# Optimization experiments

Hardware: AMD Instinct MI355X
Metric: run time of the kernel (lower is better)

The kernel has to match this reference:

```python
import jax, jax.numpy as jnp
import numpy as np
from jax.scipy.special import logsumexp

WORD_DIM = 512
SCRF_DIM = 256
N_TAGS = 12
ALLOWED_SPAN = 8
START_ID = 10
STOP_ID = 11
SEQ_LEN = 768
N_SPANS = 96


def _compute_scores(h, Wl, bl, Wr, br, Gl, bgl, Gr, bgr, Wt, bt, transitions):
    # h: [1, L, D] already projected by Dense
    Lc, D = h.shape[1], h.shape[2]
    scores = jnp.zeros((1, Lc, Lc, D), h.dtype)
    diag = jnp.arange(Lc)
    ht = h
    scores = scores.at[:, diag, diag].set(ht)
    for sl in range(1, min(ALLOWED_SPAN, Lc)):
        l, r = ht[:, :-1], ht[:, 1:]
        h_hat = 4.0 * jax.nn.sigmoid(l @ Wl.T + bl + r @ Wr.T + br) - 2.0
        # exp/normalize over 3 gates == softmax over gate axis
        g = (l @ Gl.T + bgl + r @ Gr.T + bgr).reshape(1, Lc - sl, 3, D)
        wgt = jax.nn.softmax(g, axis=2)
        ht = wgt[:, :, 0] * h_hat + wgt[:, :, 1] * l + wgt[:, :, 2] * r
        scores = scores.at[:, diag[:Lc - sl], diag[sl:]].set(ht)
    tagsc = scores @ Wt.T + bt  # [1, L, L, T]
    # final[b,i,j,prev,tag] = tagsc[b,i,j,tag] + transitions[prev,tag]
    return tagsc[:, :, :, None, :] + transitions[None, None, None]


def _forward_pass(s5):
    # s5: [1, L, L, T, T]; semi-Markov forward algorithm, windows of width <= ALLOWED_SPAN
    Lc, T = s5.shape[1], s5.shape[3]
    A = ALLOWED_SPAN
    i0 = jnp.arange(1, Lc + 1)
    k = jnp.arange(A)
    p = i0[:, None] - A + k[None, :]              # candidate span-start positions [L, A]
    m = p >= 0                                    # valid window mask (istarts = max(0, i-A))
    x = s5[0][jnp.clip(p, 0), (i0 - 1)[:, None]]  # [L, A, T, T] span scores ending at i-1
    buf0 = jnp.full((A, T), -10000.0, s5.dtype).at[A - 1, START_ID].set(0.0)

    def step(buf, inp):
        xi, mi = inp
        # tmp[k, prev, tag] = score + logalpha[start, prev]
        tmp = jnp.where(mi[:, None, None], xi + buf[:, :, None], -1e30)
        na = logsumexp(tmp, axis=(0, 1))  # [T]
        return jnp.concatenate([buf[1:], na[None]], axis=0), na

    _, alphas = jax.lax.scan(step, buf0, (x, m))
    return alphas[-1, :STOP_ID].sum()


def _gold_score(s5, tags):
    Lc, T = s5.shape[1], s5.shape[3]
    gf = tags[:, :, 0] * (Lc * T * T) + tags[:, :, 1] * (T * T) + tags[:, :, 2] * T + tags[:, :, 3]
    return jnp.take_along_axis(s5.reshape(1, -1), gf, axis=1).sum()


def setup_inputs() -> dict:
    key = jax.random.key(0)
    ks = jax.random.split(key, 16)
    D, W3 = SCRF_DIM, 3 * SCRF_DIM
    s = 0.05
    def w(k, shape):
        return jax.random.normal(k, shape, dtype=jnp.float32) * s
    return {
        "feats": jax.random.normal(ks[0], (1, SEQ_LEN, WORD_DIM), dtype=jnp.float32),
        "tags": jax.random.randint(ks[1], (1, N_SPANS, 4), 0, N_TAGS),
        "Wd": w(ks[2], (D, WORD_DIM)), "bd": jnp.zeros((D,), jnp.float32),
        "Wl": w(ks[3], (D, D)), "bl": jnp.zeros((D,), jnp.float32),
        "Wr": w(ks[4], (D, D)), "br": jnp.zeros((D,), jnp.float32),
        "Gl": w(ks[5], (W3, D)), "bgl": jnp.zeros((W3,), jnp.float32),
        "Gr": w(ks[6], (W3, D)), "bgr": jnp.zeros((W3,), jnp.float32),
        "Wt": w(ks[7], (N_TAGS, D)), "bt": jnp.zeros((N_TAGS,), jnp.float32),
        "transitions": w(ks[8], (N_TAGS, N_TAGS)),
    }


def reference(feats, tags, Wd, bd, Wl, bl, Wr, br, Gl, bgl, Gr, bgr, Wt, bt, transitions):
    h = feats @ Wd.T + bd  # Dense: word_dim -> scrf_dim
    s5 = _compute_scores(h, Wl, bl, Wr, br, Gl, bgl, Gr, bgr, Wt, bt, transitions)
    gold = _gold_score(s5, tags)
    logZ = _forward_pass(s5)
    return logZ - gold
```

## Files before the change

### kernel.cpp

```cpp
#include <hip/hip_runtime.h>

typedef __attribute__((ext_vector_type(8))) short short8;
typedef __attribute__((ext_vector_type(4))) float f32x4;

#define TPAD 100

__device__ __forceinline__ float bf2f(short s) {
  return __uint_as_float(((unsigned)(unsigned short)s) << 16);
}
__device__ __forceinline__ unsigned short f2bf(float f) {
  unsigned u = __float_as_uint(f);
  unsigned rounding = 0x7fffu + ((u >> 16) & 1u);
  return (unsigned short)((u + rounding) >> 16);
}

__device__ __forceinline__ void stg_f32(float* p, float v) {
  asm volatile("global_store_dword %0, %1, off sc1" :: "v"(p), "v"(v) : "memory");
}
__device__ __forceinline__ void stg_u16(unsigned short* p, unsigned short v) {
  unsigned w = v;
  asm volatile("global_store_short %0, %1, off sc1" :: "v"(p), "v"(w) : "memory");
}

#define NFLAGS 18432
__device__ __forceinline__ void flag_spin(unsigned* f, unsigned tgt) {
  unsigned n = 0;
  while (__hip_atomic_load(f, __ATOMIC_RELAXED, __HIP_MEMORY_SCOPE_AGENT) < tgt) {
    __builtin_amdgcn_s_sleep(2);
    if (++n > 2000000u) break;
  }
}
#define DRAIN() asm volatile("s_waitcnt vmcnt(0) lgkmcnt(0)" ::: "memory")

union __align__(16) SmemU {
  struct { unsigned short As[64][72]; unsigned short Ws[64][72]; float Cs[64][64]; } g;
  struct { unsigned short rows[2][8][264]; float sred[2][96]; float smu[2]; } bn;
  struct { float Bs[96 * TPAD]; float Acs[96 * TPAD]; float red[8]; } t;
  struct { float Qs[2][96 * TPAD]; float vv[4][96]; float red[8]; float redm[4]; } f;
};

__global__ void prep_kernel(const float* __restrict__ feats, const float* __restrict__ Wd,
                            const float* __restrict__ Wl, const float* __restrict__ Wr,
                            const float* __restrict__ Gl, const float* __restrict__ Gr,
                            const float* __restrict__ bl, const float* __restrict__ br,
                            const float* __restrict__ bgl, const float* __restrict__ bgr,
                            unsigned short* __restrict__ featsB, unsigned short* __restrict__ WdB,
                            unsigned short* __restrict__ WcB, float* __restrict__ bc,
                            unsigned* __restrict__ flags)
{
  int idx = blockIdx.x * 256 + threadIdx.x;
  if (idx < 393216) {
    featsB[idx] = f2bf(feats[idx]);
  } else if (idx < 524288) {
    int j = idx - 393216;
    WdB[j] = f2bf(Wd[j]);
  } else if (idx < 1048576) {
    int j = idx - 524288;
    int o = j >> 9, k = j & 511;
    float v;
    if (k < 256) v = (o < 256) ? Wl[o*256 + k] : Gl[(o-256)*256 + k];
    else { int k2 = k - 256; v = (o < 256) ? Wr[o*256 + k2] : Gr[(o-256)*256 + k2]; }
    WcB[j] = f2bf(v);
  } else if (idx < 1049600) {
    int o = idx - 1048576;
    bc[o] = (o < 256) ? bl[o] + br[o] : bgl[o-256] + bgr[o-256];
  } else {
    int j = idx - 1049600;
    if (j < NFLAGS) flags[j] = 0u;
  }
}

__device__ __forceinline__ void treelevel(SmemU& sm,
    const float* Tin, const float* Cin, float* Tout, float* Cout)
{
  const int bid = blockIdx.x;
  const int tid = threadIdx.x;
  const int wv = tid >> 6, lane = tid & 63;
  const int j = bid >> 1;
  const int cs = (bid & 1) * 48;
  const float* Ag = Tin + (size_t)(2*j) * 9216;
  const float* Bg = Tin + (size_t)(2*j + 1) * 9216;

  float4 av[9], bv[9];
  const float* ap = Ag + tid * 36;
  const float* bp = Bg + tid * 36;
  #pragma unroll
  for (int q = 0; q < 9; ++q) av[q] = *(const float4*)(ap + q*4);
  #pragma unroll
  for (int q = 0; q < 9; ++q) bv[q] = *(const float4*)(bp + q*4);
  float ma = 0.f, mb = 0.f;
  #pragma unroll
  for (int q = 0; q < 9; ++q) {
    ma = fmaxf(ma, fmaxf(fmaxf(av[q].x, av[q].y), fmaxf(av[q].z, av[q].w)));
    mb = fmaxf(mb, fmaxf(fmaxf(bv[q].x, bv[q].y), fmaxf(bv[q].z, bv[q].w)));
  }
  #pragma unroll
  for (int off = 32; off; off >>= 1) {
    ma = fmaxf(ma, __shfl_down(ma, off));
    mb = fmaxf(mb, __shfl_down(mb, off));
  }
  if (lane == 0) { sm.t.red[wv] = ma; sm.t.red[4 + wv] = mb; }
  __syncthreads();
  float fa = fmaxf(fmaxf(sm.t.red[0], sm.t.red[1]), fmaxf(sm.t.red[2], sm.t.red[3]));
  float fb = fmaxf(fmaxf(sm.t.red[4], sm.t.red[5]), fmaxf(sm.t.red[6], sm.t.red[7]));
  float ia = 1.0f / fa, ib = 1.0f / fb;

  #pragma unroll
  for (int q = 0; q < 9; ++q) {
    int e = tid*36 + q*4;
    int r = e / 96, k = e - r*96;
    float4 bb = bv[q];
    bb.x *= ib; bb.y *= ib; bb.z *= ib; bb.w *= ib;
    *(float4*)&sm.t.Bs[r*TPAD + k] = bb;
    float4 aa = av[q];
    sm.t.Acs[(k+0)*TPAD + r] = aa.x * ia;
    sm.t.Acs[(k+1)*TPAD + r] = aa.y * ia;
    sm.t.Acs[(k+2)*TPAD + r] = aa.z * ia;
    sm.t.Acs[(k+3)*TPAD + r] = aa.w * ia;
  }
  __syncthreads();

  int tr = tid >> 4, tc = tid & 15;
  int r0 = tr * 6, c0 = cs + tc * 3;
  float acc[6][3];
  #pragma unroll
  for (int i = 0; i < 6; ++i)
    #pragma unroll
    for (int m = 0; m < 3; ++m) acc[i][m] = 0.f;
  for (int k = 0; k < 96; k += 4) {
    float4 a0 = *(const float4*)&sm.t.Acs[(c0+0)*TPAD + k];
    float4 a1 = *(const float4*)&sm.t.Acs[(c0+1)*TPAD + k];
    float4 a2 = *(const float4*)&sm.t.Acs[(c0+2)*TPAD + k];
    #pragma unroll
    for (int i = 0; i < 6; ++i) {
      float4 b = *(const float4*)&sm.t.Bs[(r0+i)*TPAD + k];
      acc[i][0] += b.x*a0.x + b.y*a0.y + b.z*a0.z + b.w*a0.w;
      acc[i][1] += b.x*a1.x + b.y*a1.y + b.z*a1.z + b.w*a1.w;
      acc[i][2] += b.x*a2.x + b.y*a2.y + b.z*a2.z + b.w*a2.w;
    }
  }
  float* op = Tout + (size_t)j * 9216;
  #pragma unroll
  for (int i = 0; i < 6; ++i)
    #pragma unroll
    for (int m = 0; m < 3; ++m)
      stg_f32(&op[(size_t)(r0+i)*96 + c0 + m], acc[i][m]);
  if ((bid & 1) == 0 && tid == 0)
    stg_f32(&Cout[j], Cin[2*j] + Cin[2*j + 1] + __logf(fa) + __logf(fb));
}

__global__ __launch_bounds__(256, 2) void mega_kernel(
    const unsigned short* featsB, const unsigned short* WdB,
    const float* bd, const unsigned short* WcB, const float* bc,
    unsigned short* ht, const float* Wt, const float* bt,
    float* Bband, float* Xn, float* muv, const float* trans,
    const int* tags,
    float* T0, float* T1, float* T2, float* T3, float* T4,
    float* C0, float* C1, float* C2, float* C3, float* C4,
    float* out, unsigned* flags)
{
  __shared__ SmemU sm;
  const int bid = blockIdx.x;
  const int tid = threadIdx.x;
  const int wave = tid >> 6, lane = tid & 63;

  if (bid < 192) {
    const int p = bid % 12;
    if (bid < 48) {
      const int p0 = p * 64;
      const int n0 = (bid / 12) * 64;
      f32x4 acc[4];
      #pragma unroll
      for (int i = 0; i < 4; ++i)
        #pragma unroll
        for (int j = 0; j < 4; ++j) acc[i][j] = 0.f;
      const int lr = tid >> 3;
      const int c8 = (tid & 7) * 8;
      for (int kt = 0; kt < 8; ++kt) {
        int kb = kt * 64;
        #pragma unroll
        for (int rr = 0; rr < 64; rr += 32) {
          int row = lr + rr;
          *(short8*)(&sm.g.As[row][c8]) = *(const short8*)(featsB + (size_t)(p0 + row)*512 + kb + c8);
          *(short8*)(&sm.g.Ws[row][c8]) = *(const short8*)(WdB + (size_t)(n0 + row)*512 + kb + c8);
        }
        __syncthreads();
        int q8 = (lane >> 4) * 8;
        #pragma unroll
        for (int kk = 0; kk < 2; ++kk) {
          short8 bfr = *(const short8*)(&sm.g.Ws[wave*16 + (lane & 15)][kk*32 + q8]);
          #pragma unroll
          for (int mt = 0; mt < 4; ++mt) {
            short8 afr = *(const short8*)(&sm.g.As[mt*16 + (lane & 15)][kk*32 + q8]);
            acc[mt] = __builtin_amdgcn_mfma_f32_16x16x32_bf16(afr, bfr, acc[mt], 0, 0, 0);
          }
        }
        __syncthreads();
      }
      int o = n0 + wave*16 + (lane & 15);
      float bias = bd[o];
      #pragma unroll
      for (int mt = 0; mt < 4; ++mt)
        #pragma unroll
        for (int r = 0; r < 4; ++r) {
          int row = p0 + mt*16 + (lane >> 4)*4 + r;
          stg_u16(&ht[row*256 + o], f2bf(acc[mt][r] + bias));
        }
      DRAIN();
      __syncthreads();
      if (tid == 0) atomicAdd(&flags[(0*12 + p)*32], 1u);
    }

    for (int sl = 1; sl <= 7; ++sl) {
      unsigned tgt = (sl == 1) ? 4u : 16u;
      if (tid == 0) {
        flag_spin(&flags[((sl-1)*12 + p)*32], tgt);
        if (p < 11) flag_spin(&flags[((sl-1)*12 + p + 1)*32], tgt);
      }
      __syncthreads();
      {
        const unsigned short* htp = ht + (size_t)(sl - 1) * 196608;
        unsigned short* htn = ht + (size_t)sl * 196608;
        const int Mvalid = 768 - sl;
        const int p0 = p * 64;
        const int n0 = (bid / 12) * 16;
        f32x4 acc[4];
        #pragma unroll
        for (int i = 0; i < 4; ++i)
          #pragma unroll
          for (int j = 0; j < 4; ++j) acc[i][j] = 0.f;
        const int lr = tid >> 3;
        const int c8 = (tid & 7) * 8;
        for (int kt = 0; kt < 8; ++kt) {
          int kb = kt * 64;
          int shift = kb >> 8;
          int kcol = kb & 255;
          #pragma unroll
          for (int rr = 0; rr < 64; rr += 32) {
            int row = lr + rr;
            int grow = p0 + row + shift; if (grow > 767) grow = 767;
            *(short8*)(&sm.g.As[row][c8]) = *(const short8*)(htp + (size_t)grow*256 + kcol + c8);
            int o = (row >> 4)*256 + n0 + (row & 15);
            *(short8*)(&sm.g.Ws[row][c8]) = *(const short8*)(WcB + (size_t)o*512 + kb + c8);
          }
          __syncthreads();
          int q8 = (lane >> 4) * 8;
          #pragma unroll
          for (int kk = 0; kk < 2; ++kk) {
            short8 bfr = *(const short8*)(&sm.g.Ws[wave*16 + (lane & 15)][kk*32 + q8]);
            #pragma unroll
            for (int mt = 0; mt < 4; ++mt) {
              short8 afr = *(const short8*)(&sm.g.As[mt*16 + (lane & 15)][kk*32 + q8]);
              acc[mt] = __builtin_amdgcn_mfma_f32_16x16x32_bf16(afr, bfr, acc[mt], 0, 0, 0);
            }
          }
          __syncthreads();
        }
        #pragma unroll
        for (int mt = 0; mt < 4; ++mt)
          #pragma unroll
          for (int r = 0; r < 4; ++r)
            sm.g.Cs[mt*16 + (lane >> 4)*4 + r][wave*16 + (lane & 15)] = acc[mt][r];
        __syncthreads();

        int dl = tid & 15;
        int d = n0 + dl;
        float bz = bc[d], b0 = bc[256 + d], b1 = bc[512 + d], b2v = bc[768 + d];
        for (int pr = tid >> 4; pr < 64; pr += 16) {
          int pw = p0 + pr;
          if (pw >= Mvalid) continue;
          float z  = sm.g.Cs[pr][dl]      + bz;
          float g0 = sm.g.Cs[pr][16 + dl] + b0;
          float g1 = sm.g.Cs[pr][32 + dl] + b1;
          float g2 = sm.g.Cs[pr][48 + dl] + b2v;
          float l = bf2f((short)htp[pw*256 + d]);
          float r = bf2f((short)htp[(pw+1)*256 + d]);
          float hh = 4.f / (1.f + __expf(-z)) - 2.f;
          float mg = fmaxf(g0, fmaxf(g1, g2));
          float e0 = __expf(g0 - mg), e1 = __expf(g1 - mg), e2 = __expf(g2 - mg);
          float inv = 1.f / (e0 + e1 + e2);
          stg_u16(&htn[pw*256 + d], f2bf((e0*hh + e1*l + e2*r) * inv));
        }
      }
      DRAIN();
      __syncthreads();
      if (tid == 0) atomicAdd(&flags[(sl*12 + p)*32], 1u);
    }
  }

  for (int task = bid; task < 384; task += 256) {
    if (tid == 0) {
      int rlo = 2*task - 7; if (rlo < 0) rlo = 0;
      int tlo = rlo >> 6, thi = (2*task + 1) >> 6;
      flag_spin(&flags[(7*12 + tlo)*32], 16u);
      if (thi != tlo) flag_spin(&flags[(7*12 + thi)*32], 16u);
    }
    __syncthreads();
    const int half = tid >> 7;
    const int t2 = tid & 127;
    const int i = 2*task + 1 + half;
    for (int q = t2; q < 256; q += 128) {
      int k = q >> 5, cc = (q & 31) * 8;
      int pr = i - 8 + k;
      short8 v;
      if (pr >= 0) {
        int slx = 7 - k;
        v = *(const short8*)(ht + ((size_t)slx*768 + pr)*256 + cc);
      } else {
        #pragma unroll
        for (int j = 0; j < 8; ++j) v[j] = 0;
      }
      *(short8*)(&sm.bn.rows[half][k][cc]) = v;
    }
    __syncthreads();
    float res = -1e30f;
    if (t2 < 96) {
      int t = t2 >> 3, k = t2 & 7;
      int pr = i - 8 + k;
      if (pr >= 0) {
        float acc = 0.f;
        for (int dch = 0; dch < 256; dch += 8) {
          float4 wa = *(const float4*)(Wt + t*256 + dch);
          float4 wb = *(const float4*)(Wt + t*256 + dch + 4);
          short8 hv = *(const short8*)(&sm.bn.rows[half][k][dch]);
          acc += wa.x*bf2f(hv[0]) + wa.y*bf2f(hv[1]) + wa.z*bf2f(hv[2]) + wa.w*bf2f(hv[3])
               + wb.x*bf2f(hv[4]) + wb.y*bf2f(hv[5]) + wb.z*bf2f(hv[6]) + wb.w*bf2f(hv[7]);
        }
        res = acc + bt[t];
      }
      stg_f32(&Bband[(size_t)i*96 + t2], res);
      sm.bn.sred[half][t2] = res;
    }
    __syncthreads();
    if (t2 < 32) {
      float m = fmaxf(sm.bn.sred[half][t2],
                 fmaxf(sm.bn.sred[half][t2+32], sm.bn.sred[half][t2+64]));
      #pragma unroll
      for (int off = 16; off; off >>= 1) m = fmaxf(m, __shfl_down(m, off));
      if (t2 == 0) { stg_f32(&muv[i], m); sm.bn.smu[half] = m; }
    }
    __syncthreads();
    if (t2 < 96) stg_f32(&Xn[(size_t)i*96 + t2], __expf(res - sm.bn.smu[half]));
    DRAIN();
    __syncthreads();
    if (tid == 0) atomicAdd(&flags[(96 + task)*32], 1u);
  }
  if (bid >= 240) return;

  {
    const int chunk = bid / 5;
    const int bxx = bid % 5;
    if (tid == 0) {
      #pragma unroll
      for (int q = 0; q < 8; ++q)
        flag_spin(&flags[(96 + 8*chunk + q)*32], 1u);
    }
    __syncthreads();
    if (bxx == 0 && tid == 0) stg_f32(&C0[chunk], 0.f);
    const int a = chunk * 16;
    const int g = lane / 12;
    const int t = lane - g * 12;
    const int cidx = bxx * 20 + wave * 5 + g;
    const bool active = (g < 5) && (cidx < 96);
    const int c = active ? cidx : 95;
    const int s = c / 12, tau = c - s * 12;
    float Etc[12];
    #pragma unroll
    for (int jj = 0; jj < 12; ++jj) Etc[jj] = __expf(trans[jj*12 + t]);
    float NA[8], V[8];
    #pragma unroll
    for (int jj = 0; jj < 8; ++jj) { NA[jj] = 0.f; V[jj] = 0.f; }
    #pragma unroll
    for (int jj = 0; jj < 8; ++jj) if (jj == s) {
      NA[jj] = (t == tau) ? 1.f : 0.f;
      V[jj]  = Etc[tau];
    }
    const int gbb = (g * 12) * 4;
    #pragma unroll
    for (int m = 1; m <= 16; ++m) {
      const float* xr = Xn + (size_t)(a + m) * 96 + t * 8;
      float4 x0 = *(const float4*)xr;
      float4 x1 = *(const float4*)(xr + 4);
      float sf = __expf(-muv[a + m]);
      float na = x0.x*V[0] + x0.y*V[1] + x0.z*V[2] + x0.w*V[3]
               + x1.x*V[4] + x1.y*V[5] + x1.z*V[6] + x1.w*V[7];
      int nai = __float_as_int(na);
      float nb[12];
      #pragma unroll
      for (int jj = 0; jj < 12; ++jj)
        nb[jj] = __int_as_float(__builtin_amdgcn_ds_bpermute(gbb + jj*4, nai));
      float pp0 = nb[0]*Etc[0] + nb[1]*Etc[1] + nb[2]*Etc[2]   + nb[3]*Etc[3];
      float pp1 = nb[4]*Etc[4] + nb[5]*Etc[5] + nb[6]*Etc[6]   + nb[7]*Etc[7];
      float pp2 = nb[8]*Etc[8] + nb[9]*Etc[9] + nb[10]*Etc[10] + nb[11]*Etc[11];
      float v = (pp0 + pp1) + pp2;
      #pragma unroll
      for (int kq = 0; kq < 7; ++kq) { NA[kq] = NA[kq+1]*sf; V[kq] = V[kq+1]*sf; }
      NA[7] = na; V[7] = v;
    }
    if (active) {
      float* dst = T0 + (size_t)chunk * 9216 + c;
      #pragma unroll
      for (int jj = 0; jj < 8; ++jj) stg_f32(&dst[(size_t)(jj*12 + t) * 96], NA[jj]);
    }
    DRAIN();
    __syncthreads();
    if (tid == 0) atomicAdd(&flags[(480 + chunk)*32], 1u);
  }
  if (bid >= 48) return;

  {
    int j = bid >> 1;
    if (tid == 0) {
      flag_spin(&flags[(480 + 2*j    )*32], 5u);
      flag_spin(&flags[(480 + 2*j + 1)*32], 5u);
    }
    __syncthreads();
    treelevel(sm, T0, C0, T1, C1);
    DRAIN(); __syncthreads();
    if (tid == 0) atomicAdd(&flags[(528 + j)*32], 1u);
  }
  if (bid >= 24) return;
  {
    int j = bid >> 1;
    if (tid == 0) {
      flag_spin(&flags[(528 + 2*j    )*32], 2u);
      flag_spin(&flags[(528 + 2*j + 1)*32], 2u);
    }
    __syncthreads();
    treelevel(sm, T1, C1, T2, C2);
    DRAIN(); __syncthreads();
    if (tid == 0) atomicAdd(&flags[(552 + j)*32], 1u);
  }
  if (bid >= 12) return;
  {
    int j = bid >> 1;
    if (tid == 0) {
      flag_spin(&flags[(552 + 2*j    )*32], 2u);
      flag_spin(&flags[(552 + 2*j + 1)*32], 2u);
    }
    __syncthreads();
    treelevel(sm, T2, C2, T3, C3);
    DRAIN(); __syncthreads();
    if (tid == 0) atomicAdd(&flags[(564 + j)*32], 1u);
  }
  if (bid >= 6) return;
  {
    int j = bid >> 1;
    if (tid == 0) {
      flag_spin(&flags[(564 + 2*j    )*32], 2u);
      flag_spin(&flags[(564 + 2*j + 1)*32], 2u);
    }
    __syncthreads();
    treelevel(sm, T3, C3, T4, C4);
    DRAIN(); __syncthreads();
    if (tid == 0) atomicAdd(&flags[(570 + j)*32], 1u);
  }
  if (bid) return;

  {
    if (tid == 0) {
      flag_spin(&flags[(570)*32], 2u);
      flag_spin(&flags[(571)*32], 2u);
      flag_spin(&flags[(572)*32], 2u);
    }
    __syncthreads();
    float4 P[9];
    const float* p0p = T4 + tid * 36;
    #pragma unroll
    for (int q = 0; q < 9; ++q) P[q] = *(const float4*)(p0p + q*4);

    float gold = 0.f;
    if (tid < 96) {
      int a = tags[tid*4+0], b = tags[tid*4+1], cc = tags[tid*4+2], d = tags[tid*4+3];
      float v = trans[cc*12 + d];
      int sl = b - a;
      if (sl >= 0 && sl < 8) v += Bband[(size_t)(b+1)*96 + d*8 + (7 - sl)];
      else v += bt[d];
      gold = v;
    }
    float mp = 0.f;
    for (int q = tid; q < 768; q += 256) mp += muv[1 + q];
    #pragma unroll
    for (int off = 32; off; off >>= 1) {
      gold += __shfl_down(gold, off);
      mp   += __shfl_down(mp, off);
    }
    if (lane == 0) { sm.f.red[wave] = gold; sm.f.red[4 + wave] = mp; }

    #pragma unroll
    for (int q = 0; q < 9; ++q) {
      int e = tid*36 + q*4;
      int r = e / 96, k = e - r*96;
      *(float4*)&sm.f.Qs[0][r*TPAD + k] = P[q];
    }
    if (tid < 96) sm.f.vv[0][tid] = (tid == 94) ? 1.f : 0.f;
    __syncthreads();
    float gold_t = sm.f.red[0] + sm.f.red[1] + sm.f.red[2] + sm.f.red[3];
    float musum  = sm.f.red[4] + sm.f.red[5] + sm.f.red[6] + sm.f.red[7];
    float Ct = C4[0] + C4[1] + C4[2];

    #pragma unroll
    for (int s = 0; s < 3; ++s) {
      if (s < 2) {
        const float* pn = T4 + (size_t)(s+1)*9216 + tid*36;
        #pragma unroll
        for (int q = 0; q < 9; ++q) P[q] = *(const float4*)(pn + q*4);
      }
      float acc = 0.f;
      if (tid < 96) {
        const float* Qr = &sm.f.Qs[s & 1][tid * TPAD];
        #pragma unroll
        for (int k = 0; k < 96; k += 4) {
          float4 qv = *(const float4*)(Qr + k);
          float4 zv = *(const float4*)&sm.f.vv[s][k];
          acc += qv.x*zv.x + qv.y*zv.y + qv.z*zv.z + qv.w*zv.w;
        }
      }
      float am = (tid < 96) ? acc : 0.f;
      #pragma unroll
      for (int off = 32; off; off >>= 1) am = fmaxf(am, __shfl_down(am, off));
      if (lane == 0) sm.f.redm[wave] = am;
      __syncthreads();
      float mx = fmaxf(fmaxf(sm.f.redm[0], sm.f.redm[1]), fmaxf(sm.f.redm[2], sm.f.redm[3]));
      Ct += __logf(mx);
      if (tid < 96) sm.f.vv[s+1][tid] = acc / mx;
      if (s < 2) {
        #pragma unroll
        for (int q = 0; q < 9; ++q) {
          int e = tid*36 + q*4;
          int r = e / 96, k = e - r*96;
          *(float4*)&sm.f.Qs[(s+1)&1][r*TPAD + k] = P[q];
        }
      }
      __syncthreads();
    }
    if (tid == 0) {
      float lsum = 0.f;
      #pragma unroll
      for (int t = 0; t < 11; ++t) lsum += __logf(sm.f.vv[3][84 + t]);
      out[0] = lsum + 11.f * (Ct + musum) - gold_t;
    }
  }
}

extern "C" void kernel_launch(void* const* d_in, const int* in_sizes, int n_in,
                              void* d_out, int out_size, void* d_ws, size_t ws_size,
                              hipStream_t stream)
{
  const float* feats = (const float*)d_in[0];
  const int*   tags  = (const int*)  d_in[1];
  const float* Wd    = (const float*)d_in[2];
  const float* bd    = (const float*)d_in[3];
  const float* Wl    = (const float*)d_in[4];
  const float* bl    = (const float*)d_in[5];
  const float* Wr    = (const float*)d_in[6];
  const float* br    = (const float*)d_in[7];
  const float* Gl    = (const float*)d_in[8];
  const float* bgl   = (const float*)d_in[9];
  const float* Gr    = (const float*)d_in[10];
  const float* bgr   = (const float*)d_in[11];
  const float* Wt    = (const float*)d_in[12];
  const float* bt    = (const float*)d_in[13];
  const float* trans = (const float*)d_in[14];
  float* out = (float*)d_out;

  char* ws = (char*)d_ws;
  unsigned short* featsB = (unsigned short*)(ws + 0);
  unsigned short* WdB    = (unsigned short*)(ws + 786432);
  unsigned short* WcB    = (unsigned short*)(ws + 1048576);
  float*          bc     = (float*)         (ws + 2097152);
  unsigned short* ht     = (unsigned short*)(ws + 2101248);
  float*          Bband  = (float*)         (ws + 5246976);
  float*          Xn     = (float*)         (ws + 5542272);
  float*          muv    = (float*)         (ws + 5837568);
  float*          T0     = (float*)         (ws + 5841664);
  float*          T1     = (float*)         (ws + 7611136);
  float*          T2     = (float*)         (ws + 8495872);
  float*          T3     = (float*)         (ws + 8938240);
  float*          T4     = (float*)         (ws + 9159424);
  float*          C0     = (float*)         (ws + 9270016);
  float*          C1     = (float*)         (ws + 9270272);
  float*          C2     = (float*)         (ws + 9270528);
  float*          C3     = (float*)         (ws + 9270784);
  float*          C4     = (float*)         (ws + 9271040);
  unsigned*       flags  = (unsigned*)      (ws + 9271296);

  prep_kernel<<<4172, 256, 0, stream>>>(feats, Wd, Wl, Wr, Gl, Gr, bl, br, bgl, bgr,
                                        featsB, WdB, WcB, bc, flags);
  mega_kernel<<<256, 256, 0, stream>>>(featsB, WdB, bd, WcB, bc, ht, Wt, bt,
                                       Bband, Xn, muv, trans, tags,
                                       T0, T1, T2, T3, T4, C0, C1, C2, C3, C4,
                                       out, flags);
}
```

Measured before the change: 219.9 us.

## Replace tree reduction of chunk matrices with sequential matrix-vector chain

Removes the multi-level tree of 96x96 matrix-matrix products (with per-level flag barriers and intermediate buffers) and instead has one block walk the 48 chunk transfer matrices sequentially, doing a matrix-vector product per chunk as each becomes ready, with prefetch of the next chunk. This trades parallel O(n^3) GEMM levels and several inter-block sync hops for a serial chain of cheap mat-vecs that can overlap with chunk production. It also vectorizes the gating epilogue to process two bf16 columns per thread with 32-bit loads/stores, and shortens the spin-wait sleep.

```diff
diff --git a/kernel.cpp b/kernel.cpp
--- a/kernel.cpp
+++ b/kernel.cpp
@@ -21,12 +21,15 @@
   unsigned w = v;
   asm volatile("global_store_short %0, %1, off sc1" :: "v"(p), "v"(w) : "memory");
 }
+__device__ __forceinline__ void stg_u32(unsigned* p, unsigned v) {
+  asm volatile("global_store_dword %0, %1, off sc1" :: "v"(p), "v"(v) : "memory");
+}
 
 #define NFLAGS 18432
 __device__ __forceinline__ void flag_spin(unsigned* f, unsigned tgt) {
   unsigned n = 0;
   while (__hip_atomic_load(f, __ATOMIC_RELAXED, __HIP_MEMORY_SCOPE_AGENT) < tgt) {
-    __builtin_amdgcn_s_sleep(2);
+    __builtin_amdgcn_s_sleep(1);
     if (++n > 2000000u) break;
   }
 }
@@ -35,8 +38,7 @@
 union __align__(16) SmemU {
   struct { unsigned short As[64][72]; unsigned short Ws[64][72]; float Cs[64][64]; } g;
   struct { unsigned short rows[2][8][264]; float sred[2][96]; float smu[2]; } bn;
-  struct { float Bs[96 * TPAD]; float Acs[96 * TPAD]; float red[8]; } t;
-  struct { float Qs[2][96 * TPAD]; float vv[4][96]; float red[8]; float redm[4]; } f;
+  struct { float Qs[2][96 * TPAD]; float vv[2][96]; float red[8]; float redm[4]; } f;
 };
 
 __global__ void prep_kernel(const float* __restrict__ feats, const float* __restrict__ Wd,
@@ -70,94 +72,12 @@
   }
 }
 
-__device__ __forceinline__ void treelevel(SmemU& sm,
-    const float* Tin, const float* Cin, float* Tout, float* Cout)
-{
-  const int bid = blockIdx.x;
-  const int tid = threadIdx.x;
-  const int wv = tid >> 6, lane = tid & 63;
-  const int j = bid >> 1;
-  const int cs = (bid & 1) * 48;
-  const float* Ag = Tin + (size_t)(2*j) * 9216;
-  const float* Bg = Tin + (size_t)(2*j + 1) * 9216;
-
-  float4 av[9], bv[9];
-  const float* ap = Ag + tid * 36;
-  const float* bp = Bg + tid * 36;
-  #pragma unroll
-  for (int q = 0; q < 9; ++q) av[q] = *(const float4*)(ap + q*4);
-  #pragma unroll
-  for (int q = 0; q < 9; ++q) bv[q] = *(const float4*)(bp + q*4);
-  float ma = 0.f, mb = 0.f;
-  #pragma unroll
-  for (int q = 0; q < 9; ++q) {
-    ma = fmaxf(ma, fmaxf(fmaxf(av[q].x, av[q].y), fmaxf(av[q].z, av[q].w)));
-    mb = fmaxf(mb, fmaxf(fmaxf(bv[q].x, bv[q].y), fmaxf(bv[q].z, bv[q].w)));
-  }
-  #pragma unroll
-  for (int off = 32; off; off >>= 1) {
-    ma = fmaxf(ma, __shfl_down(ma, off));
-    mb = fmaxf(mb, __shfl_down(mb, off));
-  }
-  if (lane == 0) { sm.t.red[wv] = ma; sm.t.red[4 + wv] = mb; }
-  __syncthreads();
-  float fa = fmaxf(fmaxf(sm.t.red[0], sm.t.red[1]), fmaxf(sm.t.red[2], sm.t.red[3]));
-  float fb = fmaxf(fmaxf(sm.t.red[4], sm.t.red[5]), fmaxf(sm.t.red[6], sm.t.red[7]));
-  float ia = 1.0f / fa, ib = 1.0f / fb;
-
-  #pragma unroll
-  for (int q = 0; q < 9; ++q) {
-    int e = tid*36 + q*4;
-    int r = e / 96, k = e - r*96;
-    float4 bb = bv[q];
-    bb.x *= ib; bb.y *= ib; bb.z *= ib; bb.w *= ib;
-    *(float4*)&sm.t.Bs[r*TPAD + k] = bb;
-    float4 aa = av[q];
-    sm.t.Acs[(k+0)*TPAD + r] = aa.x * ia;
-    sm.t.Acs[(k+1)*TPAD + r] = aa.y * ia;
-    sm.t.Acs[(k+2)*TPAD + r] = aa.z * ia;
-    sm.t.Acs[(k+3)*TPAD + r] = aa.w * ia;
-  }
-  __syncthreads();
-
-  int tr = tid >> 4, tc = tid & 15;
-  int r0 = tr * 6, c0 = cs + tc * 3;
-  float acc[6][3];
-  #pragma unroll
-  for (int i = 0; i < 6; ++i)
-    #pragma unroll
-    for (int m = 0; m < 3; ++m) acc[i][m] = 0.f;
-  for (int k = 0; k < 96; k += 4) {
-    float4 a0 = *(const float4*)&sm.t.Acs[(c0+0)*TPAD + k];
-    float4 a1 = *(const float4*)&sm.t.Acs[(c0+1)*TPAD + k];
-    float4 a2 = *(const float4*)&sm.t.Acs[(c0+2)*TPAD + k];
-    #pragma unroll
-    for (int i = 0; i < 6; ++i) {
-      float4 b = *(const float4*)&sm.t.Bs[(r0+i)*TPAD + k];
-      acc[i][0] += b.x*a0.x + b.y*a0.y + b.z*a0.z + b.w*a0.w;
-      acc[i][1] += b.x*a1.x + b.y*a1.y + b.z*a1.z + b.w*a1.w;
-      acc[i][2] += b.x*a2.x + b.y*a2.y + b.z*a2.z + b.w*a2.w;
-    }
-  }
-  float* op = Tout + (size_t)j * 9216;
-  #pragma unroll
-  for (int i = 0; i < 6; ++i)
-    #pragma unroll
-    for (int m = 0; m < 3; ++m)
-      stg_f32(&op[(size_t)(r0+i)*96 + c0 + m], acc[i][m]);
-  if ((bid & 1) == 0 && tid == 0)
-    stg_f32(&Cout[j], Cin[2*j] + Cin[2*j + 1] + __logf(fa) + __logf(fb));
-}
-
 __global__ __launch_bounds__(256, 2) void mega_kernel(
     const unsigned short* featsB, const unsigned short* WdB,
     const float* bd, const unsigned short* WcB, const float* bc,
     unsigned short* ht, const float* Wt, const float* bt,
     float* Bband, float* Xn, float* muv, const float* trans,
-    const int* tags,
-    float* T0, float* T1, float* T2, float* T3, float* T4,
-    float* C0, float* C1, float* C2, float* C3, float* C4,
-    float* out, unsigned* flags)
+    const int* tags, float* T0, float* out, unsigned* flags)
 {
   __shared__ SmemU sm;
   const int bid = blockIdx.x;
@@ -263,23 +183,34 @@
             sm.g.Cs[mt*16 + (lane >> 4)*4 + r][wave*16 + (lane & 15)] = acc[mt][r];
         __syncthreads();
 
-        int dl = tid & 15;
-        int d = n0 + dl;
-        float bz = bc[d], b0 = bc[256 + d], b1 = bc[512 + d], b2v = bc[768 + d];
-        for (int pr = tid >> 4; pr < 64; pr += 16) {
+        int dl = tid & 7;
+        int d0 = n0 + dl*2;
+        int cc0 = dl*2;
+        float bz0 = bc[d0],       bz1 = bc[d0+1];
+        float b00 = bc[256 + d0], b01 = bc[256 + d0 + 1];
+        float b10 = bc[512 + d0], b11 = bc[512 + d0 + 1];
+        float b20 = bc[768 + d0], b21 = bc[768 + d0 + 1];
+        for (int pr = tid >> 3; pr < 64; pr += 32) {
           int pw = p0 + pr;
           if (pw >= Mvalid) continue;
-          float z  = sm.g.Cs[pr][dl]      + bz;
-          float g0 = sm.g.Cs[pr][16 + dl] + b0;
-          float g1 = sm.g.Cs[pr][32 + dl] + b1;
-          float g2 = sm.g.Cs[pr][48 + dl] + b2v;
-          float l = bf2f((short)htp[pw*256 + d]);
-          float r = bf2f((short)htp[(pw+1)*256 + d]);
-          float hh = 4.f / (1.f + __expf(-z)) - 2.f;
-          float mg = fmaxf(g0, fmaxf(g1, g2));
-          float e0 = __expf(g0 - mg), e1 = __expf(g1 - mg), e2 = __expf(g2 - mg);
-          float inv = 1.f / (e0 + e1 + e2);
-          stg_u16(&htn[pw*256 + d], f2bf((e0*hh + e1*l + e2*r) * inv));
+          float z0 = sm.g.Cs[pr][cc0]      + bz0, z1 = sm.g.Cs[pr][cc0+1]      + bz1;
+          float g00 = sm.g.Cs[pr][16+cc0]  + b00, g01 = sm.g.Cs[pr][16+cc0+1]  + b01;
+          float g10 = sm.g.Cs[pr][32+cc0]  + b10, g11 = sm.g.Cs[pr][32+cc0+1]  + b11;
+          float g20 = sm.g.Cs[pr][48+cc0]  + b20, g21 = sm.g.Cs[pr][48+cc0+1]  + b21;
+          unsigned lv = *(const unsigned*)(htp + (size_t)pw*256 + d0);
+          unsigned rv = *(const unsigned*)(htp + (size_t)(pw+1)*256 + d0);
+          float l0 = bf2f((short)(lv & 0xffff)), l1 = bf2f((short)(lv >> 16));
+          float r0v = bf2f((short)(rv & 0xffff)), r1v = bf2f((short)(rv >> 16));
+          float hh0 = 4.f / (1.f + __expf(-z0)) - 2.f;
+          float hh1 = 4.f / (1.f + __expf(-z1)) - 2.f;
+          float mg0 = fmaxf(g00, fmaxf(g10, g20));
+          float mg1 = fmaxf(g01, fmaxf(g11, g21));
+          float e00 = __expf(g00 - mg0), e10 = __expf(g10 - mg0), e20 = __expf(g20 - mg0);
+          float e01 = __expf(g01 - mg1), e11 = __expf(g11 - mg1), e21 = __expf(g21 - mg1);
+          float o0 = (e00*hh0 + e10*l0 + e20*r0v) / (e00 + e10 + e20);
+          float o1 = (e01*hh1 + e11*l1 + e21*r1v) / (e01 + e11 + e21);
+          unsigned pack = (unsigned)f2bf(o0) | ((unsigned)f2bf(o1) << 16);
+          stg_u32((unsigned*)(htn + (size_t)pw*256 + d0), pack);
         }
       }
       DRAIN();
@@ -345,9 +276,8 @@
     __syncthreads();
     if (tid == 0) atomicAdd(&flags[(96 + task)*32], 1u);
   }
-  if (bid >= 240) return;
-
-  {
+
+  if (bid < 240) {
     const int chunk = bid / 5;
     const int bxx = bid % 5;
     if (tid == 0) {
@@ -356,7 +286,6 @@
         flag_spin(&flags[(96 + 8*chunk + q)*32], 1u);
     }
     __syncthreads();
-    if (bxx == 0 && tid == 0) stg_f32(&C0[chunk], 0.f);
     const int a = chunk * 16;
     const int g = lane / 12;
     const int t = lane - g * 12;
@@ -405,69 +334,68 @@
     DRAIN();
     __syncthreads();
     if (tid == 0) atomicAdd(&flags[(480 + chunk)*32], 1u);
-  }
-  if (bid >= 48) return;
+    return;
+  }
+  if (bid != 255) return;
 
   {
-    int j = bid >> 1;
-    if (tid == 0) {
-      flag_spin(&flags[(480 + 2*j    )*32], 5u);
-      flag_spin(&flags[(480 + 2*j + 1)*32], 5u);
-    }
-    __syncthreads();
-    treelevel(sm, T0, C0, T1, C1);
-    DRAIN(); __syncthreads();
-    if (tid == 0) atomicAdd(&flags[(528 + j)*32], 1u);
-  }
-  if (bid >= 24) return;
-  {
-    int j = bid >> 1;
-    if (tid == 0) {
-      flag_spin(&flags[(528 + 2*j    )*32], 2u);
-      flag_spin(&flags[(528 + 2*j + 1)*32], 2u);
-    }
-    __syncthreads();
-    treelevel(sm, T1, C1, T2, C2);
-    DRAIN(); __syncthreads();
-    if (tid == 0) atomicAdd(&flags[(552 + j)*32], 1u);
-  }
-  if (bid >= 12) return;
-  {
-    int j = bid >> 1;
-    if (tid == 0) {
-      flag_spin(&flags[(552 + 2*j    )*32], 2u);
-      flag_spin(&flags[(552 + 2*j + 1)*32], 2u);
-    }
-    __syncthreads();
-    treelevel(sm, T2, C2, T3, C3);
-    DRAIN(); __syncthreads();
-    if (tid == 0) atomicAdd(&flags[(564 + j)*32], 1u);
-  }
-  if (bid >= 6) return;
-  {
-    int j = bid >> 1;
-    if (tid == 0) {
-      flag_spin(&flags[(564 + 2*j    )*32], 2u);
-      flag_spin(&flags[(564 + 2*j + 1)*32], 2u);
-    }
-    __syncthreads();
-    treelevel(sm, T3, C3, T4, C4);
-    DRAIN(); __syncthreads();
-    if (tid == 0) atomicAdd(&flags[(570 + j)*32], 1u);
-  }
-  if (bid) return;
-
-  {
-    if (tid == 0) {
-      flag_spin(&flags[(570)*32], 2u);
-      flag_spin(&flags[(571)*32], 2u);
-      flag_spin(&flags[(572)*32], 2u);
-    }
-    __syncthreads();
     float4 P[9];
-    const float* p0p = T4 + tid * 36;
-    #pragma unroll
-    for (int q = 0; q < 9; ++q) P[q] = *(const float4*)(p0p + q*4);
+    if (tid == 0) flag_spin(&flags[(480 + 0)*32], 5u);
+    __syncthreads();
+    {
+      const float* p0p = T0 + tid * 36;
+      #pragma unroll
+      for (int q = 0; q < 9; ++q) P[q] = *(const float4*)(p0p + q*4);
+    }
+    #pragma unroll
+    for (int q = 0; q < 9; ++q) {
+      int e = tid*36 + q*4;
+      int r = e / 96, k = e - r*96;
+      *(float4*)&sm.f.Qs[0][r*TPAD + k] = P[q];
+    }
+    if (tid < 96) sm.f.vv[0][tid] = (tid == 94) ? 1.f : 0.f;
+    __syncthreads();
+
+    float Ct = 0.f;
+    int cur = 0;
+    for (int c = 0; c < 48; ++c) {
+      if (c < 47) {
+        if (tid == 0) flag_spin(&flags[(480 + c + 1)*32], 5u);
+        __syncthreads();
+        const float* pn = T0 + (size_t)(c+1)*9216 + tid*36;
+        #pragma unroll
+        for (int q = 0; q < 9; ++q) P[q] = *(const float4*)(pn + q*4);
+      }
+      float acc = 0.f;
+      if (tid < 96) {
+        const float* Qr = &sm.f.Qs[cur][tid * TPAD];
+        #pragma unroll
+        for (int k = 0; k < 96; k += 4) {
+          float4 qv = *(const float4*)(Qr + k);
+          float4 zv = *(const float4*)&sm.f.vv[cur][k];
+          acc += qv.x*zv.x + qv.y*zv.y + qv.z*zv.z + qv.w*zv.w;
+        }
+      }
+      float am = (tid < 96) ? acc : 0.f;
+      #pragma unroll
+      for (int off = 32; off; off >>= 1) am = fmaxf(am, __shfl_down(am, off));
+      if (lane == 0) sm.f.redm[wave] = am;
+      __syncthreads();
+      float mx = fmaxf(fmaxf(sm.f.redm[0], sm.f.redm[1]), fmaxf(sm.f.redm[2], sm.f.redm[3]));
+      Ct += __logf(mx);
+      if (tid < 96) sm.f.vv[cur ^ 1][tid] = acc / mx;
+      __syncthreads();
+      if (c < 47) {
+        #pragma unroll
+        for (int q = 0; q < 9; ++q) {
+          int e = tid*36 + q*4;
+          int r = e / 96, k = e - r*96;
+          *(float4*)&sm.f.Qs[cur ^ 1][r*TPAD + k] = P[q];
+        }
+      }
+      cur ^= 1;
+      __syncthreads();
+    }
 
     float gold = 0.f;
     if (tid < 96) {
@@ -486,58 +414,13 @@
       mp   += __shfl_down(mp, off);
     }
     if (lane == 0) { sm.f.red[wave] = gold; sm.f.red[4 + wave] = mp; }
-
-    #pragma unroll
-    for (int q = 0; q < 9; ++q) {
-      int e = tid*36 + q*4;
-      int r = e / 96, k = e - r*96;
-      *(float4*)&sm.f.Qs[0][r*TPAD + k] = P[q];
-    }
-    if (tid < 96) sm.f.vv[0][tid] = (tid == 94) ? 1.f : 0.f;
-    __syncthreads();
-    float gold_t = sm.f.red[0] + sm.f.red[1] + sm.f.red[2] + sm.f.red[3];
-    float musum  = sm.f.red[4] + sm.f.red[5] + sm.f.red[6] + sm.f.red[7];
-    float Ct = C4[0] + C4[1] + C4[2];
-
-    #pragma unroll
-    for (int s = 0; s < 3; ++s) {
-      if (s < 2) {
-        const float* pn = T4 + (size_t)(s+1)*9216 + tid*36;
-        #pragma unroll
-        for (int q = 0; q < 9; ++q) P[q] = *(const float4*)(pn + q*4);
-      }
-      float acc = 0.f;
-      if (tid < 96) {
-        const float* Qr = &sm.f.Qs[s & 1][tid * TPAD];
-        #pragma unroll
-        for (int k = 0; k < 96; k += 4) {
-          float4 qv = *(const float4*)(Qr + k);
-          float4 zv = *(const float4*)&sm.f.vv[s][k];
-          acc += qv.x*zv.x + qv.y*zv.y + qv.z*zv.z + qv.w*zv.w;
-        }
-      }
-      float am = (tid < 96) ? acc : 0.f;
-      #pragma unroll
-      for (int off = 32; off; off >>= 1) am = fmaxf(am, __shfl_down(am, off));
-      if (lane == 0) sm.f.redm[wave] = am;
-      __syncthreads();
-      float mx = fmaxf(fmaxf(sm.f.redm[0], sm.f.redm[1]), fmaxf(sm.f.redm[2], sm.f.redm[3]));
-      Ct += __logf(mx);
-      if (tid < 96) sm.f.vv[s+1][tid] = acc / mx;
-      if (s < 2) {
-        #pragma unroll
-        for (int q = 0; q < 9; ++q) {
-          int e = tid*36 + q*4;
-          int r = e / 96, k = e - r*96;
-          *(float4*)&sm.f.Qs[(s+1)&1][r*TPAD + k] = P[q];
-        }
-      }
-      __syncthreads();
-    }
+    __syncthreads();
     if (tid == 0) {
+      float gold_t = sm.f.red[0] + sm.f.red[1] + sm.f.red[2] + sm.f.red[3];
+      float musum  = sm.f.red[4] + sm.f.red[5] + sm.f.red[6] + sm.f.red[7];
       float lsum = 0.f;
       #pragma unroll
-      for (int t = 0; t < 11; ++t) lsum += __logf(sm.f.vv[3][84 + t]);
+      for (int t = 0; t < 11; ++t) lsum += __logf(sm.f.vv[cur][84 + t]);
       out[0] = lsum + 11.f * (Ct + musum) - gold_t;
     }
   }
@@ -574,21 +457,10 @@
   float*          Xn     = (float*)         (ws + 5542272);
   float*          muv    = (float*)         (ws + 5837568);
   float*          T0     = (float*)         (ws + 5841664);
-  float*          T1     = (float*)         (ws + 7611136);
-  float*          T2     = (float*)         (ws + 8495872);
-  float*          T3     = (float*)         (ws + 8938240);
-  float*          T4     = (float*)         (ws + 9159424);
-  float*          C0     = (float*)         (ws + 9270016);
-  float*          C1     = (float*)         (ws + 9270272);
-  float*          C2     = (float*)         (ws + 9270528);
-  float*          C3     = (float*)         (ws + 9270784);
-  float*          C4     = (float*)         (ws + 9271040);
   unsigned*       flags  = (unsigned*)      (ws + 9271296);
 
   prep_kernel<<<4172, 256, 0, stream>>>(feats, Wd, Wl, Wr, Gl, Gr, bl, br, bgl, bgr,
                                         featsB, WdB, WcB, bc, flags);
   mega_kernel<<<256, 256, 0, stream>>>(featsB, WdB, bd, WcB, bc, ht, Wt, bt,
-                                       Bband, Xn, muv, trans, tags,
-                                       T0, T1, T2, T3, T4, C0, C1, C2, C3, C4,
-                                       out, flags);
-}
+                                       Bband, Xn, muv, trans, tags, T0, out, flags);
+}
```

New measurement: 335.0 us. 52.4% more time.
